# Kernel tuning notes

Hardware: AMD Instinct MI355X
Metric: run time of the kernel (lower is better)

The kernel has to match this reference:

```python
import jax, jax.numpy as jnp
import numpy as np

N = 50000   # nodes
E = 500000  # edges
G = 64      # graphs in batch
H = 2       # attention heads
D = 64      # hidden per head (hid)
F_IN = 4    # num_features
C = 5       # num_classes
NEG_SLOPE = 0.2


def setup_inputs() -> dict:
    key = jax.random.key(0)
    ks = jax.random.split(key, 24)
    inp = {
        'x': jax.random.normal(ks[0], (N, F_IN), jnp.float32),
        'edge_index': jax.random.randint(ks[1], (2, E), 0, N, dtype=jnp.int64),
        'batch': jnp.sort(jax.random.randint(ks[2], (N,), 0, G, dtype=jnp.int64)),
    }
    ins = [F_IN, H * D, H * D, H * D]
    ki = 3
    for l, fin in enumerate(ins, 1):
        s = 1.0 / np.sqrt(fin)
        inp[f'W{l}'] = s * jax.random.normal(ks[ki], (fin, H * D), jnp.float32); ki += 1
        inp[f'asrc{l}'] = 0.1 * jax.random.normal(ks[ki], (H, D), jnp.float32); ki += 1
        inp[f'adst{l}'] = 0.1 * jax.random.normal(ks[ki], (H, D), jnp.float32); ki += 1
        inp[f'b{l}'] = 0.01 * jax.random.normal(ks[ki], (H * D,), jnp.float32); ki += 1
    inp['lin_w'] = (1.0 / np.sqrt(H * D)) * jax.random.normal(ks[ki], (H * D, C), jnp.float32); ki += 1
    inp['lin_b'] = jnp.zeros((C,), jnp.float32)
    return inp


def gat_conv(x, src, dst, W, a_src, a_dst, b):
    # x: [N, Fin] -> h: [N, H, D]
    h = (x @ W).reshape(-1, H, D)
    alpha_src = jnp.sum(h * a_src, axis=-1)  # [N, H]
    alpha_dst = jnp.sum(h * a_dst, axis=-1)  # [N, H]
    e = jax.nn.leaky_relu(alpha_src[src] + alpha_dst[dst], NEG_SLOPE)  # [E, H]
    # segment softmax over incoming edges of each dst node
    e_max = jax.ops.segment_max(e, dst, num_segments=N)  # [N, H]
    e_exp = jnp.exp(e - e_max[dst])
    denom = jax.ops.segment_sum(e_exp, dst, num_segments=N)
    alpha = e_exp / (denom[dst] + 1e-16)  # [E, H]
    msg = h[src] * alpha[:, :, None]  # [E, H, D]
    out = jax.ops.segment_sum(msg, dst, num_segments=N)  # [N, H, D]
    return out.reshape(-1, H * D) + b


def reference(x, edge_index, batch,
              W1, asrc1, adst1, b1,
              W2, asrc2, adst2, b2,
              W3, asrc3, adst3, b3,
              W4, asrc4, adst4, b4,
              lin_w, lin_b):
    src, dst = edge_index[0], edge_index[1]
    h = jax.nn.relu(gat_conv(x, src, dst, W1, asrc1, adst1, b1))
    h = jax.nn.relu(gat_conv(h, src, dst, W2, asrc2, adst2, b2))
    h = jax.nn.relu(gat_conv(h, src, dst, W3, asrc3, adst3, b3))
    h = jax.nn.relu(gat_conv(h, src, dst, W4, asrc4, adst4, b4))
    # global mean pool over graphs
    sums = jax.ops.segment_sum(h, batch, num_segments=G)  # [G, 128]
    counts = jax.ops.segment_sum(jnp.ones((h.shape[0],), h.dtype), batch, num_segments=G)
    pooled = sums / jnp.maximum(counts, 1.0)[:, None]
    return jax.nn.sigmoid(pooled @ lin_w + lin_b)  # [G, C]
```

## Files before the change

kernel.cpp:

```cpp
#include <hip/hip_runtime.h>
#include <math.h>

#define NHEAD 2
#define NDIM  64
#define HD    128
#define NGRAPH 64
#define NCLS  5
#define NEG_SLOPE 0.2f

typedef __attribute__((ext_vector_type(8))) short bf16x8;
typedef __attribute__((ext_vector_type(4))) float f32x4;

static __device__ __forceinline__ unsigned short f2bf(float f) {
    unsigned int u = __float_as_uint(f);
    u = (u + 0x7fff + ((u >> 16) & 1)) >> 16;
    return (unsigned short)u;
}
static __device__ __forceinline__ float bf2f(unsigned short b) {
    return __uint_as_float((unsigned int)b << 16);
}


__global__ void k_deg(const int* __restrict__ dst, int* __restrict__ deg, int E) {
    int i = blockIdx.x * blockDim.x + threadIdx.x;
    if (i < E) atomicAdd(&deg[dst[i]], 1);
}

__global__ __launch_bounds__(256) void k_scan_local(const int* __restrict__ deg,
                                                    int* __restrict__ ptr,
                                                    int* __restrict__ bsum, int n) {
    __shared__ int wsum[4];
    const int tid = threadIdx.x, lane = tid & 63, wid = tid >> 6;
    const int base = blockIdx.x * 2048 + tid * 8;
    int v[8];
    #pragma unroll
    for (int k = 0; k < 8; ++k) {
        int i = base + k;
        v[k] = (i < n) ? deg[i] : 0;
    }
    #pragma unroll
    for (int k = 1; k < 8; ++k) v[k] += v[k - 1];
    int x = v[7];
    #pragma unroll
    for (int off = 1; off < 64; off <<= 1) {
        int t = __shfl_up(x, off, 64);
        if (lane >= off) x += t;
    }
    if (lane == 63) wsum[wid] = x;
    __syncthreads();
    int woff = 0;
    #pragma unroll
    for (int k = 0; k < 4; ++k) woff += (k < wid) ? wsum[k] : 0;
    int texcl = woff + x - v[7];
    #pragma unroll
    for (int k = 0; k < 8; ++k) {
        int i = base + k;
        if (i < n) ptr[i + 1] = texcl + v[k];
    }
    if (tid == 255) bsum[blockIdx.x] = woff + x;
    if (blockIdx.x == 0 && tid == 0) ptr[0] = 0;
}

__global__ void k_scan_bsum(int* __restrict__ bsum, int B) {
    int lane = threadIdx.x;
    int carry = 0;
    for (int base = 0; base < B; base += 64) {
        int i = base + lane;
        int v = (i < B) ? bsum[i] : 0;
        int x = v;
        #pragma unroll
        for (int off = 1; off < 64; off <<= 1) {
            int t = __shfl_up(x, off, 64);
            if (lane >= off) x += t;
        }
        if (i < B) bsum[i] = carry + x - v;
        carry += __shfl(x, 63, 64);
    }
}

__global__ __launch_bounds__(256) void k_scan_add(int* __restrict__ ptr,
                                                  const int* __restrict__ bsum, int n) {
    int off = bsum[blockIdx.x];
    if (off == 0) return;
    const int base = blockIdx.x * 2048 + threadIdx.x * 8;
    #pragma unroll
    for (int k = 0; k < 8; ++k) {
        int i = base + k;
        if (i < n) ptr[i + 1] += off;
    }
}

__global__ void k_scatter(const int* __restrict__ src, const int* __restrict__ dst,
                          const int* __restrict__ ptr, int* __restrict__ fill,
                          int* __restrict__ csr, int E) {
    int i = blockIdx.x * blockDim.x + threadIdx.x;
    if (i < E) {
        int d = dst[i];
        int pos = atomicAdd(&fill[d], 1);
        csr[ptr[d] + pos] = src[i];
    }
}


__global__ void k_prepw(const float* __restrict__ W2, const float* __restrict__ W3,
                        const float* __restrict__ W4, unsigned short* __restrict__ Wt) {
    int idx = blockIdx.x * blockDim.x + threadIdx.x;
    if (idx >= 3 * HD * HD) return;
    int l = idx / (HD * HD), rem = idx % (HD * HD);
    int n = rem >> 7, k = rem & 127;
    const float* W = (l == 0) ? W2 : (l == 1) ? W3 : W4;
    Wt[idx] = f2bf(W[k * HD + n]);
}


__global__ void k_gemm1a(const float* __restrict__ x, const float* __restrict__ W,
                         const float* __restrict__ asrc, const float* __restrict__ adst,
                         unsigned short* __restrict__ out,
                         float* __restrict__ oas, float* __restrict__ oad, int N) {
    int n = (blockIdx.x * blockDim.x + threadIdx.x) >> 6;
    int lane = threadIdx.x & 63;
    if (n >= N) return;
    float4 xv = *(const float4*)&x[n * 4];
    int c0 = lane * 2;
    float2 w0 = *(const float2*)&W[c0];
    float2 w1 = *(const float2*)&W[128 + c0];
    float2 w2 = *(const float2*)&W[256 + c0];
    float2 w3 = *(const float2*)&W[384 + c0];
    float v0 = xv.x * w0.x + xv.y * w1.x + xv.z * w2.x + xv.w * w3.x;
    float v1 = xv.x * w0.y + xv.y * w1.y + xv.z * w2.y + xv.w * w3.y;
    unsigned int pk = (unsigned int)f2bf(v0) | ((unsigned int)f2bf(v1) << 16);
    *(unsigned int*)&out[(size_t)n * HD + c0] = pk;
    float2 av = *(const float2*)&asrc[c0];
    float2 dv = *(const float2*)&adst[c0];
    float s = v0 * av.x + v1 * av.y;
    float t = v0 * dv.x + v1 * dv.y;
    #pragma unroll
    for (int off = 16; off > 0; off >>= 1) {
        s += __shfl_xor(s, off);
        t += __shfl_xor(t, off);
    }
    if ((lane & 31) == 0) {
        int head = lane >> 5;
        oas[n * 2 + head] = s;
        oad[n * 2 + head] = t;
    }
}

#define LDA 136
__global__ __launch_bounds__(256) void k_gemm_mfma(const unsigned short* __restrict__ A,
                                                   const unsigned short* __restrict__ Wt,
                                                   const float* __restrict__ asrc,
                                                   const float* __restrict__ adst,
                                                   unsigned short* __restrict__ out,
                                                   float* __restrict__ oas,
                                                   float* __restrict__ oad, int N) {
    __shared__ unsigned short As[128 * LDA];
    __shared__ unsigned short Ws[128 * LDA];
    const int tid = threadIdx.x;
    const int nbase = blockIdx.x * 128;
    const int lane = tid & 63, w = tid >> 6;
    const int l15 = lane & 15, quad = lane >> 4;
    const int koff = quad * 8;

    for (int c = tid; c < 2048; c += 256) {
        int row = c >> 4, k8 = (c & 15) << 3;
        int g = nbase + row;
        uint4 v = make_uint4(0, 0, 0, 0);
        if (g < N) v = *(const uint4*)&A[(size_t)g * HD + k8];
        *(uint4*)&As[row * LDA + k8] = v;
    }
    for (int c = tid; c < 2048; c += 256) {
        int row = c >> 4, k8 = (c & 15) << 3;
        *(uint4*)&Ws[row * LDA + k8] = *(const uint4*)&Wt[row * HD + k8];
    }
    float av[8], dv[8];
    #pragma unroll
    for (int c = 0; c < 8; ++c) {
        av[c] = asrc[c * 16 + l15];
        dv[c] = adst[c * 16 + l15];
    }
    __syncthreads();

    f32x4 acc0[8], acc1[8];
    #pragma unroll
    for (int c = 0; c < 8; ++c) { acc0[c] = (f32x4)(0.f); acc1[c] = (f32x4)(0.f); }

    const int r0 = w * 32 + l15;
    #pragma unroll
    for (int ks = 0; ks < 4; ++ks) {
        bf16x8 a0 = *(const bf16x8*)&As[r0 * LDA + ks * 32 + koff];
        bf16x8 a1 = *(const bf16x8*)&As[(r0 + 16) * LDA + ks * 32 + koff];
        #pragma unroll
        for (int c = 0; c < 8; ++c) {
            bf16x8 b = *(const bf16x8*)&Ws[(c * 16 + l15) * LDA + ks * 32 + koff];
            acc0[c] = __builtin_amdgcn_mfma_f32_16x16x32_bf16(a0, b, acc0[c], 0, 0, 0);
            acc1[c] = __builtin_amdgcn_mfma_f32_16x16x32_bf16(a1, b, acc1[c], 0, 0, 0);
        }
    }

    #pragma unroll
    for (int i = 0; i < 2; ++i) {
        int rowb = nbase + w * 32 + i * 16 + quad * 4;
        #pragma unroll
        for (int c = 0; c < 8; ++c) {
            f32x4 v = i ? acc1[c] : acc0[c];
            int col = c * 16 + l15;
            #pragma unroll
            for (int r = 0; r < 4; ++r) {
                int row = rowb + r;
                if (row < N) out[(size_t)row * HD + col] = f2bf(v[r]);
            }
        }
        #pragma unroll
        for (int r = 0; r < 4; ++r) {
            float ps0 = 0.f, ps1 = 0.f, pd0 = 0.f, pd1 = 0.f;
            #pragma unroll
            for (int c = 0; c < 4; ++c) {
                float hv = i ? acc1[c][r] : acc0[c][r];
                ps0 += hv * av[c]; pd0 += hv * dv[c];
            }
            #pragma unroll
            for (int c = 4; c < 8; ++c) {
                float hv = i ? acc1[c][r] : acc0[c][r];
                ps1 += hv * av[c]; pd1 += hv * dv[c];
            }
            #pragma unroll
            for (int off = 1; off < 16; off <<= 1) {
                ps0 += __shfl_xor(ps0, off);
                ps1 += __shfl_xor(ps1, off);
                pd0 += __shfl_xor(pd0, off);
                pd1 += __shfl_xor(pd1, off);
            }
            int row = rowb + r;
            if (l15 == 0 && row < N) {
                *(float2*)&oas[row * 2] = make_float2(ps0, ps1);
                *(float2*)&oad[row * 2] = make_float2(pd0, pd1);
            }
        }
    }
}

__global__ void k_gatheras(const float* __restrict__ oas, const int* __restrict__ csr,
                           float2* __restrict__ as_csr, int E) {
    int i = blockIdx.x * blockDim.x + threadIdx.x;
    if (i < E) {
        int s = csr[i];
        as_csr[i] = *(const float2*)&oas[s * 2];
    }
}

__global__ void k_agg(const unsigned short* __restrict__ h, const float2* __restrict__ as_csr,
                      const float* __restrict__ oad, const int* __restrict__ ptr,
                      const int* __restrict__ csr, const float* __restrict__ bias,
                      unsigned short* __restrict__ out, int N) {
    int n = (blockIdx.x * blockDim.x + threadIdx.x) >> 6;
    int lane = threadIdx.x & 63;
    if (n >= N) return;
    int beg = ptr[n], end = ptr[n + 1];
    if (beg == end) {
        float2 b2 = *(const float2*)&bias[lane * 2];
        unsigned int packed = (unsigned int)f2bf(fmaxf(b2.x, 0.f)) |
                              ((unsigned int)f2bf(fmaxf(b2.y, 0.f)) << 16);
        *(unsigned int*)&out[(size_t)n * HD + lane * 2] = packed;
        return;
    }
    const int quad = lane >> 4, sub = lane & 15;
    const int hsel = sub >> 3;
    float2 adn = *(const float2*)&oad[n * 2];
    float m0 = -INFINITY, m1 = -INFINITY, l0 = 0.f, l1 = 0.f;
    float acc[8];
    #pragma unroll
    for (int k = 0; k < 8; ++k) acc[k] = 0.f;

    for (int cbeg = beg; cbeg < end; cbeg += 64) {
        int cnt = min(64, end - cbeg);
        int s = 0;
        float e0 = -INFINITY, e1 = -INFINITY;
        if (lane < cnt) {
            s = csr[cbeg + lane];
            float2 as = as_csr[cbeg + lane];
            e0 = as.x + adn.x; e0 = (e0 >= 0.f) ? e0 : NEG_SLOPE * e0;
            e1 = as.y + adn.y; e1 = (e1 >= 0.f) ? e1 : NEG_SLOPE * e1;
        }
        float c0 = e0, c1 = e1;
        #pragma unroll
        for (int off = 32; off > 0; off >>= 1) {
            c0 = fmaxf(c0, __shfl_xor(c0, off));
            c1 = fmaxf(c1, __shfl_xor(c1, off));
        }
        float nm0 = fmaxf(m0, c0), nm1 = fmaxf(m1, c1);
        float sc0 = __expf(m0 - nm0), sc1 = __expf(m1 - nm1);
        float p0 = (lane < cnt) ? __expf(e0 - nm0) : 0.f;
        float p1 = (lane < cnt) ? __expf(e1 - nm1) : 0.f;
        float s0 = p0, s1 = p1;
        #pragma unroll
        for (int off = 32; off > 0; off >>= 1) {
            s0 += __shfl_xor(s0, off);
            s1 += __shfl_xor(s1, off);
        }
        l0 = l0 * sc0 + s0;
        l1 = l1 * sc1 + s1;
        m0 = nm0; m1 = nm1;
        float scl = hsel ? sc1 : sc0;
        #pragma unroll
        for (int k = 0; k < 8; ++k) acc[k] *= scl;

        for (int j = 0; j < cnt; j += 8) {
            int jq0 = j + quad, jq1 = j + quad + 4;
            int sa = __shfl(s, jq0);
            int sb = __shfl(s, jq1);
            float pa0 = __shfl(p0, jq0);
            float pa1 = __shfl(p1, jq0);
            float pb0 = __shfl(p0, jq1);
            float pb1 = __shfl(p1, jq1);
            float pa = hsel ? pa1 : pa0;
            float pb = hsel ? pb1 : pb0;
            uint4 hva = *(const uint4*)&h[(size_t)sa * HD + sub * 8];
            uint4 hvb = *(const uint4*)&h[(size_t)sb * HD + sub * 8];
            #pragma unroll
            for (int k = 0; k < 4; ++k) {
                unsigned int ua = (&hva.x)[k];
                unsigned int ub = (&hvb.x)[k];
                acc[2 * k]     += pa * __uint_as_float(ua << 16) + pb * __uint_as_float(ub << 16);
                acc[2 * k + 1] += pa * __uint_as_float(ua & 0xffff0000u) + pb * __uint_as_float(ub & 0xffff0000u);
            }
        }
    }
    #pragma unroll
    for (int k = 0; k < 8; ++k) {
        acc[k] += __shfl_xor(acc[k], 16);
        acc[k] += __shfl_xor(acc[k], 32);
    }
    if (quad == 0) {
        float lsel = hsel ? l1 : l0;
        float inv = 1.f / (lsel + 1e-16f);
        float4 ba = *(const float4*)&bias[sub * 8];
        float4 bb = *(const float4*)&bias[sub * 8 + 4];
        float o[8];
        o[0] = fmaxf(acc[0] * inv + ba.x, 0.f);
        o[1] = fmaxf(acc[1] * inv + ba.y, 0.f);
        o[2] = fmaxf(acc[2] * inv + ba.z, 0.f);
        o[3] = fmaxf(acc[3] * inv + ba.w, 0.f);
        o[4] = fmaxf(acc[4] * inv + bb.x, 0.f);
        o[5] = fmaxf(acc[5] * inv + bb.y, 0.f);
        o[6] = fmaxf(acc[6] * inv + bb.z, 0.f);
        o[7] = fmaxf(acc[7] * inv + bb.w, 0.f);
        uint4 pk;
        pk.x = (unsigned int)f2bf(o[0]) | ((unsigned int)f2bf(o[1]) << 16);
        pk.y = (unsigned int)f2bf(o[2]) | ((unsigned int)f2bf(o[3]) << 16);
        pk.z = (unsigned int)f2bf(o[4]) | ((unsigned int)f2bf(o[5]) << 16);
        pk.w = (unsigned int)f2bf(o[6]) | ((unsigned int)f2bf(o[7]) << 16);
        *(uint4*)&out[(size_t)n * HD + sub * 8] = pk;
    }
}

__global__ void k_pool(const unsigned short* __restrict__ feat, const int* __restrict__ batch,
                       float* __restrict__ pooled, int* __restrict__ gcount, int N) {
    int col = threadIdx.x;
    int n0 = blockIdx.x * 128;
    int n1 = min(n0 + 128, N);
    float acc = 0.f;
    int curg = -1, runlen = 0;
    for (int n = n0; n < n1; ++n) {
        int g = batch[n];
        if (g != curg) {
            if (curg >= 0) {
                atomicAdd(&pooled[curg * HD + col], acc);
                if (col == 0) atomicAdd(&gcount[curg], runlen);
            }
            acc = 0.f; runlen = 0;
            curg = g;
        }
        acc += bf2f(feat[(size_t)n * HD + col]);
        runlen++;
    }
    if (curg >= 0) {
        atomicAdd(&pooled[curg * HD + col], acc);
        if (col == 0) atomicAdd(&gcount[curg], runlen);
    }
}

__global__ void k_final(const float* __restrict__ pooled, const int* __restrict__ gcount,
                        const float* __restrict__ lw, const float* __restrict__ lb,
                        float* __restrict__ out) {
    int tid = threadIdx.x;
    if (tid >= NGRAPH * NCLS) return;
    int g = tid / NCLS, c = tid % NCLS;
    float cnt = fmaxf((float)gcount[g], 1.f);
    const float* p = pooled + g * HD;
    float sum = 0.f;
    for (int k = 0; k < HD; ++k)
        sum += p[k] * lw[k * NCLS + c];
    float z = lb[c] + sum / cnt;
    out[tid] = 1.f / (1.f + __expf(-z));
}


static inline size_t al256(size_t x) { return (x + 255) & ~(size_t)255; }

extern "C" void kernel_launch(void* const* d_in, const int* in_sizes, int n_in,
                              void* d_out, int out_size, void* d_ws, size_t ws_size,
                              hipStream_t stream) {
    const int N = in_sizes[0] / 4;
    const int E = in_sizes[1] / 2;

    const float* x     = (const float*)d_in[0];
    const int*   esrc  = (const int*)d_in[1];
    const int*   edst  = esrc + E;
    const int*   batch = (const int*)d_in[2];
    const float* Wl[4]  = {(const float*)d_in[3],  (const float*)d_in[7],
                           (const float*)d_in[11], (const float*)d_in[15]};
    const float* asr[4] = {(const float*)d_in[4],  (const float*)d_in[8],
                           (const float*)d_in[12], (const float*)d_in[16]};
    const float* ads[4] = {(const float*)d_in[5],  (const float*)d_in[9],
                           (const float*)d_in[13], (const float*)d_in[17]};
    const float* bs[4]  = {(const float*)d_in[6],  (const float*)d_in[10],
                           (const float*)d_in[14], (const float*)d_in[18]};
    const float* lin_w = (const float*)d_in[19];
    const float* lin_b = (const float*)d_in[20];
    float* out = (float*)d_out;

    char* w = (char*)d_ws;
    size_t off = 0;
    auto alloc = [&](size_t bytes) -> void* {
        void* p = w + off;
        off = al256(off + bytes);
        return p;
    };
    int*   deg    = (int*)alloc((size_t)N * 4);
    int*   fill   = (int*)alloc((size_t)N * 4);
    int*   gcount = (int*)alloc((size_t)NGRAPH * 4);
    float* pooled = (float*)alloc((size_t)NGRAPH * HD * 4);
    size_t zbytes = off;
    int*   ptr    = (int*)alloc((size_t)(N + 1) * 4);
    int*   bsum   = (int*)alloc((size_t)1024 * 4);
    int*   csr    = (int*)alloc((size_t)E * 4);
    unsigned short* hbuf = (unsigned short*)alloc((size_t)N * HD * 2);
    unsigned short* feat = (unsigned short*)alloc((size_t)N * HD * 2);
    unsigned short* Wt   = (unsigned short*)alloc((size_t)3 * HD * HD * 2);
    float*  a_src  = (float*)alloc((size_t)N * 2 * 4);
    float*  a_dst  = (float*)alloc((size_t)N * 2 * 4);
    float2* as_csr = (float2*)alloc((size_t)E * 8);
    (void)ws_size; (void)n_in; (void)out_size;

    hipMemsetAsync(d_ws, 0, zbytes, stream);

    k_prepw<<<(3 * HD * HD + 255) / 256, 256, 0, stream>>>(Wl[1], Wl[2], Wl[3], Wt);
    k_deg<<<(E + 255) / 256, 256, 0, stream>>>(edst, deg, E);
    const int SB = (N + 2047) / 2048;
    k_scan_local<<<SB, 256, 0, stream>>>(deg, ptr, bsum, N);
    k_scan_bsum<<<1, 64, 0, stream>>>(bsum, SB);
    k_scan_add<<<SB, 256, 0, stream>>>(ptr, bsum, N);
    k_scatter<<<(E + 255) / 256, 256, 0, stream>>>(esrc, edst, ptr, fill, csr, E);

    const int node_wave_blocks = (N + 3) / 4;
    const int edge_blocks = (E + 255) / 256;

    for (int layer = 0; layer < 4; ++layer) {
        if (layer == 0) {
            k_gemm1a<<<node_wave_blocks, 256, 0, stream>>>(
                x, Wl[0], asr[0], ads[0], hbuf, a_src, a_dst, N);
        } else {
            k_gemm_mfma<<<(N + 127) / 128, 256, 0, stream>>>(
                feat, Wt + (size_t)(layer - 1) * HD * HD,
                asr[layer], ads[layer], hbuf, a_src, a_dst, N);
        }
        k_gatheras<<<edge_blocks, 256, 0, stream>>>(a_src, csr, as_csr, E);
        k_agg<<<node_wave_blocks, 256, 0, stream>>>(hbuf, as_csr, a_dst, ptr, csr, bs[layer], feat, N);
    }

    k_pool<<<(N + 127) / 128, 128, 0, stream>>>(feat, batch, pooled, gcount, N);
    k_final<<<1, 320, 0, stream>>>(pooled, gcount, lin_w, lin_b, out);
}
```

Baseline: 414.8 us.

## Fuse whole GAT pipeline into one persistent cooperative kernel with grid syncs

Replaces the sequence of roughly twenty kernel launches with a single cooperative persistent kernel that walks CSR build, the four GAT layers, pooling and the final linear layer, separated by grid-wide barriers. The aggregation step now gathers source attention scores straight from a_src by CSR index instead of going through a separate gather kernel and as_csr buffer, and the GEMM reads A directly from global memory rather than staging it in LDS. It also merges the degree count with the weight preparation in the fallback path. The aim is to remove launch gaps and intermediate traffic, at the cost of grid.sync overhead, a fixed grid size limited by occupancy, and a gather per edge for attention scores.

```diff
diff --git a/kernel.cpp b/kernel.cpp
--- a/kernel.cpp
+++ b/kernel.cpp
@@ -1,5 +1,8 @@
 #include <hip/hip_runtime.h>
+#include <hip/hip_cooperative_groups.h>
 #include <math.h>
+
+namespace cg = cooperative_groups;
 
 #define NHEAD 2
 #define NDIM  64
@@ -7,6 +10,9 @@
 #define NGRAPH 64
 #define NCLS  5
 #define NEG_SLOPE 0.2f
+#define LDA   136
+#define BLK   256
+#define TOTAL_CU 256
 
 typedef __attribute__((ext_vector_type(8))) short bf16x8;
 typedef __attribute__((ext_vector_type(4))) float f32x4;
@@ -20,10 +26,430 @@
     return __uint_as_float((unsigned int)b << 16);
 }
 
-
-__global__ void k_deg(const int* __restrict__ dst, int* __restrict__ deg, int E) {
-    int i = blockIdx.x * blockDim.x + threadIdx.x;
-    if (i < E) atomicAdd(&deg[dst[i]], 1);
+struct MegaP {
+    const float* x;
+    const int*   esrc;
+    const int*   edst;
+    const int*   batch;
+    const float *W1, *as1, *ad1, *b1;
+    const float *W2, *as2, *ad2, *b2;
+    const float *W3, *as3, *ad3, *b3;
+    const float *W4, *as4, *ad4, *b4;
+    const float *lin_w, *lin_b;
+    float* out;
+    int *deg, *fill, *gcount;
+    float* pooled;
+    int *ptr, *bsum, *csr;
+    unsigned short *hbuf, *feat, *Wt;
+    float *a_src, *a_dst;
+    int N, E, SB;
+};
+
+
+static __device__ void prepw_body(const float* __restrict__ W2, const float* __restrict__ W3,
+                                  const float* __restrict__ W4, unsigned short* __restrict__ Wt,
+                                  int gtid, int nthreads) {
+    for (int idx = gtid; idx < 3 * HD * HD; idx += nthreads) {
+        int l = idx / (HD * HD), rem = idx % (HD * HD);
+        int nn = rem >> 7, k = rem & 127;
+        const float* W = (l == 0) ? W2 : (l == 1) ? W3 : W4;
+        Wt[idx] = f2bf(W[k * HD + nn]);
+    }
+}
+
+static __device__ void gemm1a_body(const float* __restrict__ x, const float* __restrict__ W,
+                                   const float* __restrict__ asrc, const float* __restrict__ adst,
+                                   unsigned short* __restrict__ out,
+                                   float* __restrict__ oas, float* __restrict__ oad,
+                                   int N, int gwave, int nwaves, int lane) {
+    int c0 = lane * 2;
+    float2 w0 = *(const float2*)&W[c0];
+    float2 w1 = *(const float2*)&W[128 + c0];
+    float2 w2 = *(const float2*)&W[256 + c0];
+    float2 w3 = *(const float2*)&W[384 + c0];
+    float2 av = *(const float2*)&asrc[c0];
+    float2 dv = *(const float2*)&adst[c0];
+    for (int n = gwave; n < N; n += nwaves) {
+        float4 xv = *(const float4*)&x[n * 4];
+        float v0 = xv.x * w0.x + xv.y * w1.x + xv.z * w2.x + xv.w * w3.x;
+        float v1 = xv.x * w0.y + xv.y * w1.y + xv.z * w2.y + xv.w * w3.y;
+        unsigned int pk = (unsigned int)f2bf(v0) | ((unsigned int)f2bf(v1) << 16);
+        *(unsigned int*)&out[(size_t)n * HD + c0] = pk;
+        float s = v0 * av.x + v1 * av.y;
+        float t = v0 * dv.x + v1 * dv.y;
+        #pragma unroll
+        for (int off = 16; off > 0; off >>= 1) {
+            s += __shfl_xor(s, off);
+            t += __shfl_xor(t, off);
+        }
+        if ((lane & 31) == 0) {
+            int head = lane >> 5;
+            oas[n * 2 + head] = s;
+            oad[n * 2 + head] = t;
+        }
+    }
+}
+
+static __device__ void gemm_body(const unsigned short* __restrict__ A,
+                                 const unsigned short* __restrict__ Wt,
+                                 const float* __restrict__ asrc, const float* __restrict__ adst,
+                                 unsigned short* __restrict__ out,
+                                 float* __restrict__ oas, float* __restrict__ oad,
+                                 int N, unsigned short* Ws, int bid, int nblocks, int tid) {
+    const int lane = tid & 63, w = tid >> 6;
+    const int l15 = lane & 15, quad = lane >> 4;
+    const int koff = quad * 8;
+    for (int c = tid; c < 2048; c += BLK) {
+        int row = c >> 4, k8 = (c & 15) << 3;
+        *(uint4*)&Ws[row * LDA + k8] = *(const uint4*)&Wt[row * HD + k8];
+    }
+    float av[8], dv[8];
+    #pragma unroll
+    for (int c = 0; c < 8; ++c) {
+        av[c] = asrc[c * 16 + l15];
+        dv[c] = adst[c * 16 + l15];
+    }
+    __syncthreads();
+
+    const int ntiles = (N + 127) >> 7;
+    for (int tile = bid; tile < ntiles; tile += nblocks) {
+        const int nbase = tile * 128;
+        f32x4 acc0[8], acc1[8];
+        #pragma unroll
+        for (int c = 0; c < 8; ++c) { acc0[c] = (f32x4)(0.f); acc1[c] = (f32x4)(0.f); }
+        const int r0 = nbase + w * 32 + l15;
+        const int r1 = r0 + 16;
+        #pragma unroll
+        for (int ks = 0; ks < 4; ++ks) {
+            bf16x8 a0 = (bf16x8)(short)0, a1 = (bf16x8)(short)0;
+            if (r0 < N) a0 = *(const bf16x8*)&A[(size_t)r0 * HD + ks * 32 + koff];
+            if (r1 < N) a1 = *(const bf16x8*)&A[(size_t)r1 * HD + ks * 32 + koff];
+            #pragma unroll
+            for (int c = 0; c < 8; ++c) {
+                bf16x8 b = *(const bf16x8*)&Ws[(c * 16 + l15) * LDA + ks * 32 + koff];
+                acc0[c] = __builtin_amdgcn_mfma_f32_16x16x32_bf16(a0, b, acc0[c], 0, 0, 0);
+                acc1[c] = __builtin_amdgcn_mfma_f32_16x16x32_bf16(a1, b, acc1[c], 0, 0, 0);
+            }
+        }
+        #pragma unroll
+        for (int i = 0; i < 2; ++i) {
+            int rowb = nbase + w * 32 + i * 16 + quad * 4;
+            #pragma unroll
+            for (int c = 0; c < 8; ++c) {
+                f32x4 v = i ? acc1[c] : acc0[c];
+                int col = c * 16 + l15;
+                #pragma unroll
+                for (int r = 0; r < 4; ++r) {
+                    int row = rowb + r;
+                    if (row < N) out[(size_t)row * HD + col] = f2bf(v[r]);
+                }
+            }
+            #pragma unroll
+            for (int r = 0; r < 4; ++r) {
+                float ps0 = 0.f, ps1 = 0.f, pd0 = 0.f, pd1 = 0.f;
+                #pragma unroll
+                for (int c = 0; c < 4; ++c) {
+                    float hv = i ? acc1[c][r] : acc0[c][r];
+                    ps0 += hv * av[c]; pd0 += hv * dv[c];
+                }
+                #pragma unroll
+                for (int c = 4; c < 8; ++c) {
+                    float hv = i ? acc1[c][r] : acc0[c][r];
+                    ps1 += hv * av[c]; pd1 += hv * dv[c];
+                }
+                #pragma unroll
+                for (int off = 1; off < 16; off <<= 1) {
+                    ps0 += __shfl_xor(ps0, off);
+                    ps1 += __shfl_xor(ps1, off);
+                    pd0 += __shfl_xor(pd0, off);
+                    pd1 += __shfl_xor(pd1, off);
+                }
+                int row = rowb + r;
+                if (l15 == 0 && row < N) {
+                    *(float2*)&oas[row * 2] = make_float2(ps0, ps1);
+                    *(float2*)&oad[row * 2] = make_float2(pd0, pd1);
+                }
+            }
+        }
+    }
+}
+
+static __device__ void agg_body(const unsigned short* __restrict__ h,
+                                const float* __restrict__ oas, const float* __restrict__ oad,
+                                const int* __restrict__ ptr, const int* __restrict__ csr,
+                                const float* __restrict__ bias,
+                                unsigned short* __restrict__ out,
+                                int N, int gwave, int nwaves, int lane) {
+    const int quad = lane >> 4, sub = lane & 15;
+    const int hsel = sub >> 3;
+    float2 b2 = *(const float2*)&bias[lane * 2];
+    float4 ba = *(const float4*)&bias[sub * 8];
+    float4 bb = *(const float4*)&bias[sub * 8 + 4];
+    unsigned int piso = (unsigned int)f2bf(fmaxf(b2.x, 0.f)) |
+                        ((unsigned int)f2bf(fmaxf(b2.y, 0.f)) << 16);
+
+    for (int n = gwave; n < N; n += nwaves) {
+        int beg = ptr[n], end = ptr[n + 1];
+        if (beg == end) {
+            *(unsigned int*)&out[(size_t)n * HD + lane * 2] = piso;
+            continue;
+        }
+        float2 adn = *(const float2*)&oad[n * 2];
+        float m0 = -INFINITY, m1 = -INFINITY, l0 = 0.f, l1 = 0.f;
+        float acc[8];
+        #pragma unroll
+        for (int k = 0; k < 8; ++k) acc[k] = 0.f;
+
+        for (int cbeg = beg; cbeg < end; cbeg += 64) {
+            int cnt = min(64, end - cbeg);
+            int s = 0;
+            float e0 = -INFINITY, e1 = -INFINITY;
+            if (lane < cnt) {
+                s = csr[cbeg + lane];
+                float2 as = *(const float2*)&oas[s * 2];
+                e0 = as.x + adn.x; e0 = (e0 >= 0.f) ? e0 : NEG_SLOPE * e0;
+                e1 = as.y + adn.y; e1 = (e1 >= 0.f) ? e1 : NEG_SLOPE * e1;
+            }
+            float c0 = e0, c1 = e1;
+            #pragma unroll
+            for (int off = 32; off > 0; off >>= 1) {
+                c0 = fmaxf(c0, __shfl_xor(c0, off));
+                c1 = fmaxf(c1, __shfl_xor(c1, off));
+            }
+            float nm0 = fmaxf(m0, c0), nm1 = fmaxf(m1, c1);
+            float sc0 = __expf(m0 - nm0), sc1 = __expf(m1 - nm1);
+            float p0 = (lane < cnt) ? __expf(e0 - nm0) : 0.f;
+            float p1 = (lane < cnt) ? __expf(e1 - nm1) : 0.f;
+            float s0 = p0, s1 = p1;
+            #pragma unroll
+            for (int off = 32; off > 0; off >>= 1) {
+                s0 += __shfl_xor(s0, off);
+                s1 += __shfl_xor(s1, off);
+            }
+            l0 = l0 * sc0 + s0;
+            l1 = l1 * sc1 + s1;
+            m0 = nm0; m1 = nm1;
+            float scl = hsel ? sc1 : sc0;
+            #pragma unroll
+            for (int k = 0; k < 8; ++k) acc[k] *= scl;
+
+            for (int j = 0; j < cnt; j += 8) {
+                int jq0 = j + quad, jq1 = j + quad + 4;
+                int sa = __shfl(s, jq0);
+                int sb = __shfl(s, jq1);
+                float pa0 = __shfl(p0, jq0);
+                float pa1 = __shfl(p1, jq0);
+                float pb0 = __shfl(p0, jq1);
+                float pb1 = __shfl(p1, jq1);
+                float pa = hsel ? pa1 : pa0;
+                float pb = hsel ? pb1 : pb0;
+                uint4 hva = *(const uint4*)&h[(size_t)sa * HD + sub * 8];
+                uint4 hvb = *(const uint4*)&h[(size_t)sb * HD + sub * 8];
+                #pragma unroll
+                for (int k = 0; k < 4; ++k) {
+                    unsigned int ua = (&hva.x)[k];
+                    unsigned int ub = (&hvb.x)[k];
+                    acc[2 * k]     += pa * __uint_as_float(ua << 16) + pb * __uint_as_float(ub << 16);
+                    acc[2 * k + 1] += pa * __uint_as_float(ua & 0xffff0000u) + pb * __uint_as_float(ub & 0xffff0000u);
+                }
+            }
+        }
+        #pragma unroll
+        for (int k = 0; k < 8; ++k) {
+            acc[k] += __shfl_xor(acc[k], 16);
+            acc[k] += __shfl_xor(acc[k], 32);
+        }
+        if (quad == 0) {
+            float lsel = hsel ? l1 : l0;
+            float inv = 1.f / (lsel + 1e-16f);
+            float o[8];
+            o[0] = fmaxf(acc[0] * inv + ba.x, 0.f);
+            o[1] = fmaxf(acc[1] * inv + ba.y, 0.f);
+            o[2] = fmaxf(acc[2] * inv + ba.z, 0.f);
+            o[3] = fmaxf(acc[3] * inv + ba.w, 0.f);
+            o[4] = fmaxf(acc[4] * inv + bb.x, 0.f);
+            o[5] = fmaxf(acc[5] * inv + bb.y, 0.f);
+            o[6] = fmaxf(acc[6] * inv + bb.z, 0.f);
+            o[7] = fmaxf(acc[7] * inv + bb.w, 0.f);
+            uint4 pk;
+            pk.x = (unsigned int)f2bf(o[0]) | ((unsigned int)f2bf(o[1]) << 16);
+            pk.y = (unsigned int)f2bf(o[2]) | ((unsigned int)f2bf(o[3]) << 16);
+            pk.z = (unsigned int)f2bf(o[4]) | ((unsigned int)f2bf(o[5]) << 16);
+            pk.w = (unsigned int)f2bf(o[6]) | ((unsigned int)f2bf(o[7]) << 16);
+            *(uint4*)&out[(size_t)n * HD + sub * 8] = pk;
+        }
+    }
+}
+
+static __device__ void pool_body(const unsigned short* __restrict__ feat,
+                                 const int* __restrict__ batch,
+                                 float* __restrict__ pooled, int* __restrict__ gcount,
+                                 int N, int bid, int nblocks, int tid) {
+    int ptiles = (N + 255) >> 8;
+    int col = tid & 127, half = tid >> 7;
+    for (int tb = bid; tb < ptiles; tb += nblocks) {
+        int n0 = tb * 256 + half * 128;
+        int n1 = min(n0 + 128, N);
+        float acc = 0.f;
+        int curg = -1, runlen = 0;
+        for (int n = n0; n < n1; ++n) {
+            int g = batch[n];
+            if (g != curg) {
+                if (curg >= 0) {
+                    atomicAdd(&pooled[curg * HD + col], acc);
+                    if (col == 0) atomicAdd(&gcount[curg], runlen);
+                }
+                acc = 0.f; runlen = 0;
+                curg = g;
+            }
+            acc += bf2f(feat[(size_t)n * HD + col]);
+            runlen++;
+        }
+        if (curg >= 0) {
+            atomicAdd(&pooled[curg * HD + col], acc);
+            if (col == 0) atomicAdd(&gcount[curg], runlen);
+        }
+    }
+}
+
+static __device__ void final_body(const float* __restrict__ pooled, const int* __restrict__ gcount,
+                                  const float* __restrict__ lw, const float* __restrict__ lb,
+                                  float* __restrict__ out, int tid) {
+    if (tid < NGRAPH) {
+        float cnt = fmaxf((float)gcount[tid], 1.f);
+        const float* pl = pooled + tid * HD;
+        #pragma unroll
+        for (int c = 0; c < NCLS; ++c) {
+            float sum = 0.f;
+            for (int k = 0; k < HD; ++k)
+                sum += pl[k] * lw[k * NCLS + c];
+            float z = lb[c] + sum / cnt;
+            out[tid * NCLS + c] = 1.f / (1.f + __expf(-z));
+        }
+    }
+}
+
+__global__ __launch_bounds__(BLK, 4) void k_mega(MegaP p) {
+    cg::grid_group grid = cg::this_grid();
+    __shared__ unsigned short Ws[128 * LDA];
+    __shared__ int wsum[4];
+    const int tid = threadIdx.x, bid = blockIdx.x, nblocks = gridDim.x;
+    const int gtid = bid * BLK + tid;
+    const int nthreads = nblocks * BLK;
+    const int lane = tid & 63;
+    const int gwave = gtid >> 6, nwaves = nthreads >> 6;
+    const int N = p.N, E = p.E;
+
+    prepw_body(p.W2, p.W3, p.W4, p.Wt, gtid, nthreads);
+    for (int i = gtid; i < E; i += nthreads) atomicAdd(&p.deg[p.edst[i]], 1);
+    gemm1a_body(p.x, p.W1, p.as1, p.ad1, p.hbuf, p.a_src, p.a_dst, N, gwave, nwaves, lane);
+    grid.sync();
+
+    for (int tb = bid; tb < p.SB; tb += nblocks) {
+        const int wid = tid >> 6;
+        const int base = tb * 2048 + tid * 8;
+        int v[8];
+        #pragma unroll
+        for (int k = 0; k < 8; ++k) {
+            int i = base + k;
+            v[k] = (i < N) ? p.deg[i] : 0;
+        }
+        #pragma unroll
+        for (int k = 1; k < 8; ++k) v[k] += v[k - 1];
+        int x = v[7];
+        #pragma unroll
+        for (int off = 1; off < 64; off <<= 1) {
+            int t = __shfl_up(x, off, 64);
+            if (lane >= off) x += t;
+        }
+        if (lane == 63) wsum[wid] = x;
+        __syncthreads();
+        int woff = 0;
+        #pragma unroll
+        for (int k = 0; k < 4; ++k) woff += (k < wid) ? wsum[k] : 0;
+        int texcl = woff + x - v[7];
+        #pragma unroll
+        for (int k = 0; k < 8; ++k) {
+            int i = base + k;
+            if (i < N) p.ptr[i + 1] = texcl + v[k];
+        }
+        if (tid == 255) p.bsum[tb] = woff + x;
+        __syncthreads();
+    }
+    if (bid == 0 && tid == 0) p.ptr[0] = 0;
+    grid.sync();
+
+    if (bid == 0 && tid < 64) {
+        int v = (tid < p.SB) ? p.bsum[tid] : 0;
+        int x = v;
+        #pragma unroll
+        for (int off = 1; off < 64; off <<= 1) {
+            int t = __shfl_up(x, off, 64);
+            if (tid >= off) x += t;
+        }
+        if (tid < p.SB) p.bsum[tid] = x - v;
+    }
+    grid.sync();
+
+    for (int tb = bid; tb < p.SB; tb += nblocks) {
+        int off = p.bsum[tb];
+        if (off != 0) {
+            const int base = tb * 2048 + tid * 8;
+            #pragma unroll
+            for (int k = 0; k < 8; ++k) {
+                int i = base + k;
+                if (i < N) p.ptr[i + 1] += off;
+            }
+        }
+    }
+    grid.sync();
+
+    for (int i = gtid; i < E; i += nthreads) {
+        int d = p.edst[i];
+        int pos = atomicAdd(&p.fill[d], 1);
+        p.csr[p.ptr[d] + pos] = p.esrc[i];
+    }
+    grid.sync();
+
+    agg_body(p.hbuf, p.a_src, p.a_dst, p.ptr, p.csr, p.b1, p.feat, N, gwave, nwaves, lane);
+    grid.sync();
+    gemm_body(p.feat, p.Wt, p.as2, p.ad2, p.hbuf, p.a_src, p.a_dst, N, Ws, bid, nblocks, tid);
+    grid.sync();
+    agg_body(p.hbuf, p.a_src, p.a_dst, p.ptr, p.csr, p.b2, p.feat, N, gwave, nwaves, lane);
+    grid.sync();
+    gemm_body(p.feat, p.Wt + HD * HD, p.as3, p.ad3, p.hbuf, p.a_src, p.a_dst, N, Ws, bid, nblocks, tid);
+    grid.sync();
+    agg_body(p.hbuf, p.a_src, p.a_dst, p.ptr, p.csr, p.b3, p.feat, N, gwave, nwaves, lane);
+    grid.sync();
+    gemm_body(p.feat, p.Wt + 2 * HD * HD, p.as4, p.ad4, p.hbuf, p.a_src, p.a_dst, N, Ws, bid, nblocks, tid);
+    grid.sync();
+    agg_body(p.hbuf, p.a_src, p.a_dst, p.ptr, p.csr, p.b4, p.feat, N, gwave, nwaves, lane);
+    grid.sync();
+
+    pool_body(p.feat, p.batch, p.pooled, p.gcount, N, bid, nblocks, tid);
+    grid.sync();
+
+    if (bid == 0) final_body(p.pooled, p.gcount, p.lin_w, p.lin_b, p.out, tid);
+}
+
+
+__global__ void k_deg_prepw(const int* __restrict__ dst, int* __restrict__ deg, int E,
+                            int edge_blocks,
+                            const float* __restrict__ W2, const float* __restrict__ W3,
+                            const float* __restrict__ W4, unsigned short* __restrict__ Wt) {
+    int b = blockIdx.x;
+    if (b < edge_blocks) {
+        int i = b * 256 + threadIdx.x;
+        if (i < E) atomicAdd(&deg[dst[i]], 1);
+    } else {
+        int idx = (b - edge_blocks) * 256 + threadIdx.x;
+        if (idx < 3 * HD * HD) {
+            int l = idx / (HD * HD), rem = idx % (HD * HD);
+            int nn = rem >> 7, k = rem & 127;
+            const float* W = (l == 0) ? W2 : (l == 1) ? W3 : W4;
+            Wt[idx] = f2bf(W[k * HD + nn]);
+        }
+    }
 }
 
 __global__ __launch_bounds__(256) void k_scan_local(const int* __restrict__ deg,
@@ -101,298 +527,37 @@
     }
 }
 
-
-__global__ void k_prepw(const float* __restrict__ W2, const float* __restrict__ W3,
-                        const float* __restrict__ W4, unsigned short* __restrict__ Wt) {
-    int idx = blockIdx.x * blockDim.x + threadIdx.x;
-    if (idx >= 3 * HD * HD) return;
-    int l = idx / (HD * HD), rem = idx % (HD * HD);
-    int n = rem >> 7, k = rem & 127;
-    const float* W = (l == 0) ? W2 : (l == 1) ? W3 : W4;
-    Wt[idx] = f2bf(W[k * HD + n]);
-}
-
-
-__global__ void k_gemm1a(const float* __restrict__ x, const float* __restrict__ W,
-                         const float* __restrict__ asrc, const float* __restrict__ adst,
-                         unsigned short* __restrict__ out,
-                         float* __restrict__ oas, float* __restrict__ oad, int N) {
-    int n = (blockIdx.x * blockDim.x + threadIdx.x) >> 6;
-    int lane = threadIdx.x & 63;
-    if (n >= N) return;
-    float4 xv = *(const float4*)&x[n * 4];
-    int c0 = lane * 2;
-    float2 w0 = *(const float2*)&W[c0];
-    float2 w1 = *(const float2*)&W[128 + c0];
-    float2 w2 = *(const float2*)&W[256 + c0];
-    float2 w3 = *(const float2*)&W[384 + c0];
-    float v0 = xv.x * w0.x + xv.y * w1.x + xv.z * w2.x + xv.w * w3.x;
-    float v1 = xv.x * w0.y + xv.y * w1.y + xv.z * w2.y + xv.w * w3.y;
-    unsigned int pk = (unsigned int)f2bf(v0) | ((unsigned int)f2bf(v1) << 16);
-    *(unsigned int*)&out[(size_t)n * HD + c0] = pk;
-    float2 av = *(const float2*)&asrc[c0];
-    float2 dv = *(const float2*)&adst[c0];
-    float s = v0 * av.x + v1 * av.y;
-    float t = v0 * dv.x + v1 * dv.y;
-    #pragma unroll
-    for (int off = 16; off > 0; off >>= 1) {
-        s += __shfl_xor(s, off);
-        t += __shfl_xor(t, off);
-    }
-    if ((lane & 31) == 0) {
-        int head = lane >> 5;
-        oas[n * 2 + head] = s;
-        oad[n * 2 + head] = t;
-    }
-}
-
-#define LDA 136
-__global__ __launch_bounds__(256) void k_gemm_mfma(const unsigned short* __restrict__ A,
-                                                   const unsigned short* __restrict__ Wt,
-                                                   const float* __restrict__ asrc,
-                                                   const float* __restrict__ adst,
-                                                   unsigned short* __restrict__ out,
-                                                   float* __restrict__ oas,
-                                                   float* __restrict__ oad, int N) {
-    __shared__ unsigned short As[128 * LDA];
+__global__ void k_gemm1a_w(const float* x, const float* W, const float* asrc,
+                           const float* adst, unsigned short* out,
+                           float* oas, float* oad, int N) {
+    int gwave = (blockIdx.x * blockDim.x + threadIdx.x) >> 6;
+    int nwaves = (gridDim.x * blockDim.x) >> 6;
+    gemm1a_body(x, W, asrc, adst, out, oas, oad, N, gwave, nwaves, threadIdx.x & 63);
+}
+
+__global__ __launch_bounds__(256) void k_gemm_w(const unsigned short* A, const unsigned short* Wt,
+                                                const float* asrc, const float* adst,
+                                                unsigned short* out, float* oas, float* oad, int N) {
     __shared__ unsigned short Ws[128 * LDA];
-    const int tid = threadIdx.x;
-    const int nbase = blockIdx.x * 128;
-    const int lane = tid & 63, w = tid >> 6;
-    const int l15 = lane & 15, quad = lane >> 4;
-    const int koff = quad * 8;
-
-    for (int c = tid; c < 2048; c += 256) {
-        int row = c >> 4, k8 = (c & 15) << 3;
-        int g = nbase + row;
-        uint4 v = make_uint4(0, 0, 0, 0);
-        if (g < N) v = *(const uint4*)&A[(size_t)g * HD + k8];
-        *(uint4*)&As[row * LDA + k8] = v;
-    }
-    for (int c = tid; c < 2048; c += 256) {
-        int row = c >> 4, k8 = (c & 15) << 3;
-        *(uint4*)&Ws[row * LDA + k8] = *(const uint4*)&Wt[row * HD + k8];
-    }
-    float av[8], dv[8];
-    #pragma unroll
-    for (int c = 0; c < 8; ++c) {
-        av[c] = asrc[c * 16 + l15];
-        dv[c] = adst[c * 16 + l15];
-    }
-    __syncthreads();
-
-    f32x4 acc0[8], acc1[8];
-    #pragma unroll
-    for (int c = 0; c < 8; ++c) { acc0[c] = (f32x4)(0.f); acc1[c] = (f32x4)(0.f); }
-
-    const int r0 = w * 32 + l15;
-    #pragma unroll
-    for (int ks = 0; ks < 4; ++ks) {
-        bf16x8 a0 = *(const bf16x8*)&As[r0 * LDA + ks * 32 + koff];
-        bf16x8 a1 = *(const bf16x8*)&As[(r0 + 16) * LDA + ks * 32 + koff];
-        #pragma unroll
-        for (int c = 0; c < 8; ++c) {
-            bf16x8 b = *(const bf16x8*)&Ws[(c * 16 + l15) * LDA + ks * 32 + koff];
-            acc0[c] = __builtin_amdgcn_mfma_f32_16x16x32_bf16(a0, b, acc0[c], 0, 0, 0);
-            acc1[c] = __builtin_amdgcn_mfma_f32_16x16x32_bf16(a1, b, acc1[c], 0, 0, 0);
-        }
-    }
-
-    #pragma unroll
-    for (int i = 0; i < 2; ++i) {
-        int rowb = nbase + w * 32 + i * 16 + quad * 4;
-        #pragma unroll
-        for (int c = 0; c < 8; ++c) {
-            f32x4 v = i ? acc1[c] : acc0[c];
-            int col = c * 16 + l15;
-            #pragma unroll
-            for (int r = 0; r < 4; ++r) {
-                int row = rowb + r;
-                if (row < N) out[(size_t)row * HD + col] = f2bf(v[r]);
-            }
-        }
-        #pragma unroll
-        for (int r = 0; r < 4; ++r) {
-            float ps0 = 0.f, ps1 = 0.f, pd0 = 0.f, pd1 = 0.f;
-            #pragma unroll
-            for (int c = 0; c < 4; ++c) {
-                float hv = i ? acc1[c][r] : acc0[c][r];
-                ps0 += hv * av[c]; pd0 += hv * dv[c];
-            }
-            #pragma unroll
-            for (int c = 4; c < 8; ++c) {
-                float hv = i ? acc1[c][r] : acc0[c][r];
-                ps1 += hv * av[c]; pd1 += hv * dv[c];
-            }
-            #pragma unroll
-            for (int off = 1; off < 16; off <<= 1) {
-                ps0 += __shfl_xor(ps0, off);
-                ps1 += __shfl_xor(ps1, off);
-                pd0 += __shfl_xor(pd0, off);
-                pd1 += __shfl_xor(pd1, off);
-            }
-            int row = rowb + r;
-            if (l15 == 0 && row < N) {
-                *(float2*)&oas[row * 2] = make_float2(ps0, ps1);
-                *(float2*)&oad[row * 2] = make_float2(pd0, pd1);
-            }
-        }
-    }
-}
-
-__global__ void k_gatheras(const float* __restrict__ oas, const int* __restrict__ csr,
-                           float2* __restrict__ as_csr, int E) {
-    int i = blockIdx.x * blockDim.x + threadIdx.x;
-    if (i < E) {
-        int s = csr[i];
-        as_csr[i] = *(const float2*)&oas[s * 2];
-    }
-}
-
-__global__ void k_agg(const unsigned short* __restrict__ h, const float2* __restrict__ as_csr,
-                      const float* __restrict__ oad, const int* __restrict__ ptr,
-                      const int* __restrict__ csr, const float* __restrict__ bias,
-                      unsigned short* __restrict__ out, int N) {
-    int n = (blockIdx.x * blockDim.x + threadIdx.x) >> 6;
-    int lane = threadIdx.x & 63;
-    if (n >= N) return;
-    int beg = ptr[n], end = ptr[n + 1];
-    if (beg == end) {
-        float2 b2 = *(const float2*)&bias[lane * 2];
-        unsigned int packed = (unsigned int)f2bf(fmaxf(b2.x, 0.f)) |
-                              ((unsigned int)f2bf(fmaxf(b2.y, 0.f)) << 16);
-        *(unsigned int*)&out[(size_t)n * HD + lane * 2] = packed;
-        return;
-    }
-    const int quad = lane >> 4, sub = lane & 15;
-    const int hsel = sub >> 3;
-    float2 adn = *(const float2*)&oad[n * 2];
-    float m0 = -INFINITY, m1 = -INFINITY, l0 = 0.f, l1 = 0.f;
-    float acc[8];
-    #pragma unroll
-    for (int k = 0; k < 8; ++k) acc[k] = 0.f;
-
-    for (int cbeg = beg; cbeg < end; cbeg += 64) {
-        int cnt = min(64, end - cbeg);
-        int s = 0;
-        float e0 = -INFINITY, e1 = -INFINITY;
-        if (lane < cnt) {
-            s = csr[cbeg + lane];
-            float2 as = as_csr[cbeg + lane];
-            e0 = as.x + adn.x; e0 = (e0 >= 0.f) ? e0 : NEG_SLOPE * e0;
-            e1 = as.y + adn.y; e1 = (e1 >= 0.f) ? e1 : NEG_SLOPE * e1;
-        }
-        float c0 = e0, c1 = e1;
-        #pragma unroll
-        for (int off = 32; off > 0; off >>= 1) {
-            c0 = fmaxf(c0, __shfl_xor(c0, off));
-            c1 = fmaxf(c1, __shfl_xor(c1, off));
-        }
-        float nm0 = fmaxf(m0, c0), nm1 = fmaxf(m1, c1);
-        float sc0 = __expf(m0 - nm0), sc1 = __expf(m1 - nm1);
-        float p0 = (lane < cnt) ? __expf(e0 - nm0) : 0.f;
-        float p1 = (lane < cnt) ? __expf(e1 - nm1) : 0.f;
-        float s0 = p0, s1 = p1;
-        #pragma unroll
-        for (int off = 32; off > 0; off >>= 1) {
-            s0 += __shfl_xor(s0, off);
-            s1 += __shfl_xor(s1, off);
-        }
-        l0 = l0 * sc0 + s0;
-        l1 = l1 * sc1 + s1;
-        m0 = nm0; m1 = nm1;
-        float scl = hsel ? sc1 : sc0;
-        #pragma unroll
-        for (int k = 0; k < 8; ++k) acc[k] *= scl;
-
-        for (int j = 0; j < cnt; j += 8) {
-            int jq0 = j + quad, jq1 = j + quad + 4;
-            int sa = __shfl(s, jq0);
-            int sb = __shfl(s, jq1);
-            float pa0 = __shfl(p0, jq0);
-            float pa1 = __shfl(p1, jq0);
-            float pb0 = __shfl(p0, jq1);
-            float pb1 = __shfl(p1, jq1);
-            float pa = hsel ? pa1 : pa0;
-            float pb = hsel ? pb1 : pb0;
-            uint4 hva = *(const uint4*)&h[(size_t)sa * HD + sub * 8];
-            uint4 hvb = *(const uint4*)&h[(size_t)sb * HD + sub * 8];
-            #pragma unroll
-            for (int k = 0; k < 4; ++k) {
-                unsigned int ua = (&hva.x)[k];
-                unsigned int ub = (&hvb.x)[k];
-                acc[2 * k]     += pa * __uint_as_float(ua << 16) + pb * __uint_as_float(ub << 16);
-                acc[2 * k + 1] += pa * __uint_as_float(ua & 0xffff0000u) + pb * __uint_as_float(ub & 0xffff0000u);
-            }
-        }
-    }
-    #pragma unroll
-    for (int k = 0; k < 8; ++k) {
-        acc[k] += __shfl_xor(acc[k], 16);
-        acc[k] += __shfl_xor(acc[k], 32);
-    }
-    if (quad == 0) {
-        float lsel = hsel ? l1 : l0;
-        float inv = 1.f / (lsel + 1e-16f);
-        float4 ba = *(const float4*)&bias[sub * 8];
-        float4 bb = *(const float4*)&bias[sub * 8 + 4];
-        float o[8];
-        o[0] = fmaxf(acc[0] * inv + ba.x, 0.f);
-        o[1] = fmaxf(acc[1] * inv + ba.y, 0.f);
-        o[2] = fmaxf(acc[2] * inv + ba.z, 0.f);
-        o[3] = fmaxf(acc[3] * inv + ba.w, 0.f);
-        o[4] = fmaxf(acc[4] * inv + bb.x, 0.f);
-        o[5] = fmaxf(acc[5] * inv + bb.y, 0.f);
-        o[6] = fmaxf(acc[6] * inv + bb.z, 0.f);
-        o[7] = fmaxf(acc[7] * inv + bb.w, 0.f);
-        uint4 pk;
-        pk.x = (unsigned int)f2bf(o[0]) | ((unsigned int)f2bf(o[1]) << 16);
-        pk.y = (unsigned int)f2bf(o[2]) | ((unsigned int)f2bf(o[3]) << 16);
-        pk.z = (unsigned int)f2bf(o[4]) | ((unsigned int)f2bf(o[5]) << 16);
-        pk.w = (unsigned int)f2bf(o[6]) | ((unsigned int)f2bf(o[7]) << 16);
-        *(uint4*)&out[(size_t)n * HD + sub * 8] = pk;
-    }
-}
-
-__global__ void k_pool(const unsigned short* __restrict__ feat, const int* __restrict__ batch,
-                       float* __restrict__ pooled, int* __restrict__ gcount, int N) {
-    int col = threadIdx.x;
-    int n0 = blockIdx.x * 128;
-    int n1 = min(n0 + 128, N);
-    float acc = 0.f;
-    int curg = -1, runlen = 0;
-    for (int n = n0; n < n1; ++n) {
-        int g = batch[n];
-        if (g != curg) {
-            if (curg >= 0) {
-                atomicAdd(&pooled[curg * HD + col], acc);
-                if (col == 0) atomicAdd(&gcount[curg], runlen);
-            }
-            acc = 0.f; runlen = 0;
-            curg = g;
-        }
-        acc += bf2f(feat[(size_t)n * HD + col]);
-        runlen++;
-    }
-    if (curg >= 0) {
-        atomicAdd(&pooled[curg * HD + col], acc);
-        if (col == 0) atomicAdd(&gcount[curg], runlen);
-    }
-}
-
-__global__ void k_final(const float* __restrict__ pooled, const int* __restrict__ gcount,
-                        const float* __restrict__ lw, const float* __restrict__ lb,
-                        float* __restrict__ out) {
-    int tid = threadIdx.x;
-    if (tid >= NGRAPH * NCLS) return;
-    int g = tid / NCLS, c = tid % NCLS;
-    float cnt = fmaxf((float)gcount[g], 1.f);
-    const float* p = pooled + g * HD;
-    float sum = 0.f;
-    for (int k = 0; k < HD; ++k)
-        sum += p[k] * lw[k * NCLS + c];
-    float z = lb[c] + sum / cnt;
-    out[tid] = 1.f / (1.f + __expf(-z));
+    gemm_body(A, Wt, asrc, adst, out, oas, oad, N, Ws, blockIdx.x, gridDim.x, threadIdx.x);
+}
+
+__global__ void k_agg_w(const unsigned short* h, const float* oas, const float* oad,
+                        const int* ptr, const int* csr, const float* bias,
+                        unsigned short* out, int N) {
+    int gwave = (blockIdx.x * blockDim.x + threadIdx.x) >> 6;
+    int nwaves = (gridDim.x * blockDim.x) >> 6;
+    agg_body(h, oas, oad, ptr, csr, bias, out, N, gwave, nwaves, threadIdx.x & 63);
+}
+
+__global__ void k_pool_w(const unsigned short* feat, const int* batch,
+                         float* pooled, int* gcount, int N) {
+    pool_body(feat, batch, pooled, gcount, N, blockIdx.x, gridDim.x, threadIdx.x);
+}
+
+__global__ void k_final_w(const float* pooled, const int* gcount,
+                          const float* lw, const float* lb, float* out) {
+    final_body(pooled, gcount, lw, lb, out, threadIdx.x);
 }
 
 
@@ -404,71 +569,89 @@
     const int N = in_sizes[0] / 4;
     const int E = in_sizes[1] / 2;
 
-    const float* x     = (const float*)d_in[0];
-    const int*   esrc  = (const int*)d_in[1];
-    const int*   edst  = esrc + E;
-    const int*   batch = (const int*)d_in[2];
-    const float* Wl[4]  = {(const float*)d_in[3],  (const float*)d_in[7],
-                           (const float*)d_in[11], (const float*)d_in[15]};
-    const float* asr[4] = {(const float*)d_in[4],  (const float*)d_in[8],
-                           (const float*)d_in[12], (const float*)d_in[16]};
-    const float* ads[4] = {(const float*)d_in[5],  (const float*)d_in[9],
-                           (const float*)d_in[13], (const float*)d_in[17]};
-    const float* bs[4]  = {(const float*)d_in[6],  (const float*)d_in[10],
-                           (const float*)d_in[14], (const float*)d_in[18]};
-    const float* lin_w = (const float*)d_in[19];
-    const float* lin_b = (const float*)d_in[20];
-    float* out = (float*)d_out;
+    MegaP p;
+    p.x     = (const float*)d_in[0];
+    p.esrc  = (const int*)d_in[1];
+    p.edst  = p.esrc + E;
+    p.batch = (const int*)d_in[2];
+    p.W1 = (const float*)d_in[3];  p.as1 = (const float*)d_in[4];
+    p.ad1 = (const float*)d_in[5]; p.b1 = (const float*)d_in[6];
+    p.W2 = (const float*)d_in[7];  p.as2 = (const float*)d_in[8];
+    p.ad2 = (const float*)d_in[9]; p.b2 = (const float*)d_in[10];
+    p.W3 = (const float*)d_in[11]; p.as3 = (const float*)d_in[12];
+    p.ad3 = (const float*)d_in[13]; p.b3 = (const float*)d_in[14];
+    p.W4 = (const float*)d_in[15]; p.as4 = (const float*)d_in[16];
+    p.ad4 = (const float*)d_in[17]; p.b4 = (const float*)d_in[18];
+    p.lin_w = (const float*)d_in[19];
+    p.lin_b = (const float*)d_in[20];
+    p.out = (float*)d_out;
 
     char* w = (char*)d_ws;
     size_t off = 0;
     auto alloc = [&](size_t bytes) -> void* {
-        void* p = w + off;
+        void* ptr_ = w + off;
         off = al256(off + bytes);
-        return p;
+        return ptr_;
     };
-    int*   deg    = (int*)alloc((size_t)N * 4);
-    int*   fill   = (int*)alloc((size_t)N * 4);
-    int*   gcount = (int*)alloc((size_t)NGRAPH * 4);
-    float* pooled = (float*)alloc((size_t)NGRAPH * HD * 4);
+    p.deg    = (int*)alloc((size_t)N * 4);
+    p.fill   = (int*)alloc((size_t)N * 4);
+    p.gcount = (int*)alloc((size_t)NGRAPH * 4);
+    p.pooled = (float*)alloc((size_t)NGRAPH * HD * 4);
     size_t zbytes = off;
-    int*   ptr    = (int*)alloc((size_t)(N + 1) * 4);
-    int*   bsum   = (int*)alloc((size_t)1024 * 4);
-    int*   csr    = (int*)alloc((size_t)E * 4);
-    unsigned short* hbuf = (unsigned short*)alloc((size_t)N * HD * 2);
-    unsigned short* feat = (unsigned short*)alloc((size_t)N * HD * 2);
-    unsigned short* Wt   = (unsigned short*)alloc((size_t)3 * HD * HD * 2);
-    float*  a_src  = (float*)alloc((size_t)N * 2 * 4);
-    float*  a_dst  = (float*)alloc((size_t)N * 2 * 4);
-    float2* as_csr = (float2*)alloc((size_t)E * 8);
+    p.ptr    = (int*)alloc((size_t)(N + 1) * 4);
+    p.bsum   = (int*)alloc((size_t)1024 * 4);
+    p.csr    = (int*)alloc((size_t)E * 4);
+    p.hbuf   = (unsigned short*)alloc((size_t)N * HD * 2);
+    p.feat   = (unsigned short*)alloc((size_t)N * HD * 2);
+    p.Wt     = (unsigned short*)alloc((size_t)3 * HD * HD * 2);
+    p.a_src  = (float*)alloc((size_t)N * 2 * 4);
+    p.a_dst  = (float*)alloc((size_t)N * 2 * 4);
+    p.N = N; p.E = E; p.SB = (N + 2047) / 2048;
     (void)ws_size; (void)n_in; (void)out_size;
 
     hipMemsetAsync(d_ws, 0, zbytes, stream);
 
-    k_prepw<<<(3 * HD * HD + 255) / 256, 256, 0, stream>>>(Wl[1], Wl[2], Wl[3], Wt);
-    k_deg<<<(E + 255) / 256, 256, 0, stream>>>(edst, deg, E);
-    const int SB = (N + 2047) / 2048;
-    k_scan_local<<<SB, 256, 0, stream>>>(deg, ptr, bsum, N);
-    k_scan_bsum<<<1, 64, 0, stream>>>(bsum, SB);
-    k_scan_add<<<SB, 256, 0, stream>>>(ptr, bsum, N);
-    k_scatter<<<(E + 255) / 256, 256, 0, stream>>>(esrc, edst, ptr, fill, csr, E);
-
-    const int node_wave_blocks = (N + 3) / 4;
-    const int edge_blocks = (E + 255) / 256;
-
-    for (int layer = 0; layer < 4; ++layer) {
-        if (layer == 0) {
-            k_gemm1a<<<node_wave_blocks, 256, 0, stream>>>(
-                x, Wl[0], asr[0], ads[0], hbuf, a_src, a_dst, N);
-        } else {
-            k_gemm_mfma<<<(N + 127) / 128, 256, 0, stream>>>(
-                feat, Wt + (size_t)(layer - 1) * HD * HD,
-                asr[layer], ads[layer], hbuf, a_src, a_dst, N);
-        }
-        k_gatheras<<<edge_blocks, 256, 0, stream>>>(a_src, csr, as_csr, E);
-        k_agg<<<node_wave_blocks, 256, 0, stream>>>(hbuf, as_csr, a_dst, ptr, csr, bs[layer], feat, N);
-    }
-
-    k_pool<<<(N + 127) / 128, 128, 0, stream>>>(feat, batch, pooled, gcount, N);
-    k_final<<<1, 320, 0, stream>>>(pooled, gcount, lin_w, lin_b, out);
-}
+    bool coop_ok = false;
+    int occ = 0;
+    if (hipOccupancyMaxActiveBlocksPerMultiprocessor(&occ, k_mega, BLK, 0) == hipSuccess
+        && occ > 0) {
+        int grid = occ * TOTAL_CU;
+        if (grid > 4096) grid = 4096;
+        void* args[] = { &p };
+        coop_ok = (hipLaunchCooperativeKernel(k_mega, dim3(grid), dim3(BLK), args,
+                                              0u, stream) == hipSuccess);
+    }
+
+    if (!coop_ok) {
+        const int edge_blocks = (E + 255) / 256;
+        const int prepw_blocks = (3 * HD * HD + 255) / 256;
+        k_deg_prepw<<<edge_blocks + prepw_blocks, 256, 0, stream>>>(
+            p.edst, p.deg, E, edge_blocks, p.W2, p.W3, p.W4, p.Wt);
+        k_scan_local<<<p.SB, 256, 0, stream>>>(p.deg, p.ptr, p.bsum, N);
+        k_scan_bsum<<<1, 64, 0, stream>>>(p.bsum, p.SB);
+        k_scan_add<<<p.SB, 256, 0, stream>>>(p.ptr, p.bsum, N);
+        k_scatter<<<edge_blocks, 256, 0, stream>>>(p.esrc, p.edst, p.ptr, p.fill, p.csr, E);
+
+        const int node_wave_blocks = (N + 3) / 4;
+        const float* asr[4] = {p.as1, p.as2, p.as3, p.as4};
+        const float* ads[4] = {p.ad1, p.ad2, p.ad3, p.ad4};
+        const float* bs[4]  = {p.b1, p.b2, p.b3, p.b4};
+        unsigned short* bufs[2] = {p.hbuf, p.feat};
+        for (int layer = 0; layer < 4; ++layer) {
+            unsigned short* hin  = bufs[0];
+            unsigned short* hout = bufs[1];
+            if (layer == 0) {
+                k_gemm1a_w<<<node_wave_blocks, 256, 0, stream>>>(
+                    p.x, p.W1, asr[0], ads[0], hin, p.a_src, p.a_dst, N);
+            } else {
+                k_gemm_w<<<(N + 127) / 128, 256, 0, stream>>>(
+                    hout, p.Wt + (size_t)(layer - 1) * HD * HD,
+                    asr[layer], ads[layer], hin, p.a_src, p.a_dst, N);
+            }
+            k_agg_w<<<node_wave_blocks, 256, 0, stream>>>(
+                hin, p.a_src, p.a_dst, p.ptr, p.csr, bs[layer], hout, N);
+        }
+        k_pool_w<<<(N + 255) / 256, 256, 0, stream>>>(p.feat, p.batch, p.pooled, p.gcount, N);
+        k_final_w<<<1, 64, 0, stream>>>(p.pooled, p.gcount, p.lin_w, p.lin_b, p.out);
+    }
+}
```

After: 484.7 us. 1.17x slower.
